# Optimization experiments

Hardware: AMD Instinct MI355X
Metric: run time of the kernel (lower is better)

## Reference

```python
import jax, jax.numpy as jnp
import numpy as np

EMBED_DIM = 1024
N_HEADS = 16
KV_SIZE = 64
CLIP_DIST = 10
SLEN = 1024
BSZ = 8


def setup_inputs() -> dict:
    key = jax.random.key(0)
    ks = jax.random.split(key, 7)
    s = 0.02
    inputs = jax.random.normal(ks[0], (SLEN, BSZ, EMBED_DIM), dtype=jnp.float32)
    W_in = jax.random.normal(ks[1], (3 * N_HEADS * KV_SIZE, EMBED_DIM), dtype=jnp.float32) * s
    b_in = jnp.zeros((3 * N_HEADS * KV_SIZE,), dtype=jnp.float32)
    k_dist_emb = jax.random.normal(ks[2], (CLIP_DIST + 1, KV_SIZE), dtype=jnp.float32) * s
    v_dist_emb = jax.random.normal(ks[3], (CLIP_DIST + 1, KV_SIZE), dtype=jnp.float32) * s
    W_out = jax.random.normal(ks[4], (EMBED_DIM, N_HEADS * KV_SIZE), dtype=jnp.float32) * s
    b_out = jnp.zeros((EMBED_DIM,), dtype=jnp.float32)
    return {"inputs": inputs, "W_in": W_in, "b_in": b_in,
            "k_dist_emb": k_dist_emb, "v_dist_emb": v_dist_emb,
            "W_out": W_out, "b_out": b_out}


def reference(inputs, W_in, b_in, k_dist_emb, v_dist_emb, W_out, b_out):
    slen, bsz, _ = inputs.shape
    h, d = N_HEADS, KV_SIZE
    # in_proj: (slen, bsz, 3*h*d) -> (3, bsz, h, slen, d)
    qkv = inputs @ W_in.T + b_in
    qkv = qkv.reshape(slen, bsz, 3, h, d).transpose(2, 1, 3, 0, 4)
    q, k, v = qkv[0], qkv[1], qkv[2]
    q = q * (d ** -0.5)
    # clipped absolute relative distances (slen, slen)
    idx = jnp.arange(slen)
    dist = jnp.minimum(jnp.abs(idx[None, :] - idx[:, None]), CLIP_DIST)
    k_dist = k_dist_emb[dist]  # (slen, slen, d)
    v_dist = v_dist_emb[dist]  # (slen, slen, d)
    # content scores + relative-distance bias
    attn = jnp.einsum('bhsd,bhtd->bhst', q, k) + jnp.einsum('bhsd,std->bhst', q, k_dist)
    attn = jax.nn.softmax(attn, axis=-1)
    # value accumulation + relative-distance value correction
    out = jnp.einsum('bhst,bhtd->bhsd', attn, v) + jnp.einsum('bhst,std->bhsd', attn, v_dist)
    # (bsz, h, slen, d) -> (slen, bsz, h*d)
    out = out.transpose(2, 0, 1, 3).reshape(slen, bsz, h * d)
    return out @ W_out.T + b_out
```

## Files before the change

kernel.cpp:

```cpp
#include <hip/hip_runtime.h>
#include <hip/hip_bf16.h>
#include <cstdint>


typedef __attribute__((ext_vector_type(8))) __bf16 bf16x8;
typedef __attribute__((ext_vector_type(4))) __bf16 bf16x4;
typedef __attribute__((ext_vector_type(4))) short s16x4;
typedef __attribute__((ext_vector_type(4))) float f32x4;

#if __has_builtin(__builtin_amdgcn_exp2f)
#define EXP2F(x) __builtin_amdgcn_exp2f(x)
#else
#define EXP2F(x) exp2f(x)
#endif

#if __has_builtin(__builtin_amdgcn_mfma_f32_16x16x16bf16_1k)
#define PV_MFMA(ACC, AV, BV) \
  ACC = __builtin_amdgcn_mfma_f32_16x16x16bf16_1k( \
      __builtin_bit_cast(s16x4, AV), __builtin_bit_cast(s16x4, BV), ACC, 0, 0, 0)
#elif __has_builtin(__builtin_amdgcn_mfma_f32_16x16x16_bf16)
#define PV_MFMA(ACC, AV, BV) \
  ACC = __builtin_amdgcn_mfma_f32_16x16x16_bf16(AV, BV, ACC, 0, 0, 0)
#else
#define PV_MFMA(ACC, AV, BV)                                               \
  asm volatile("s_nop 1\n\tv_mfma_f32_16x16x16_bf16 %0, %1, %2, %0\n\t"    \
               "s_nop 7\n\ts_nop 7"                                        \
               : "+v"(ACC)                                                 \
               : "v"(__builtin_bit_cast(s16x4, AV)),                       \
                 "v"(__builtin_bit_cast(s16x4, BV)))
#endif

__device__ __forceinline__ void gload_lds16(const void* g, void* l) {
  __builtin_amdgcn_global_load_lds(
      (const __attribute__((address_space(1))) void*)g,
      (__attribute__((address_space(3))) void*)l, 16, 0, 0);
}

__global__ __launch_bounds__(256) void f2b3_kernel(
    const float* __restrict__ s0, __bf16* __restrict__ d0,
    const float* __restrict__ s1, __bf16* __restrict__ d1,
    const float* __restrict__ s2, __bf16* __restrict__ d2) {
  int i = (blockIdx.x * 256 + threadIdx.x) * 8;
  const float* s; __bf16* d; int off;
  if (i < 8388608) { s = s0; d = d0; off = i; }
  else if (i < 11534336) { s = s1; d = d1; off = i - 8388608; }
  else { s = s2; d = d2; off = i - 11534336; }
  float4 a = *(const float4*)(s + off);
  float4 b = *(const float4*)(s + off + 4);
  bf16x8 o;
  o[0] = (__bf16)a.x; o[1] = (__bf16)a.y; o[2] = (__bf16)a.z; o[3] = (__bf16)a.w;
  o[4] = (__bf16)b.x; o[5] = (__bf16)b.y; o[6] = (__bf16)b.z; o[7] = (__bf16)b.w;
  *(bf16x8*)(d + off) = o;
}

template <int EPI>
__global__ __launch_bounds__(256) void gemm_nt(
    const __bf16* __restrict__ A, const __bf16* __restrict__ B,
    const float* __restrict__ bias, int K,
    float* __restrict__ outF, __bf16* __restrict__ outT, int N, int NT, int CPX) {
  __shared__ __align__(16) __bf16 sA[2][128 * 64];
  __shared__ __align__(16) __bf16 sB[2][128 * 64];
  const int tid = threadIdx.x;
  const int wave = tid >> 6, lane = tid & 63;
  const int lg = lane >> 4, lr = lane & 15;
  const int wr = wave >> 1, wc = wave & 1;
  const int lid = (blockIdx.x & 7) * CPX + (blockIdx.x >> 3);
  const int m0 = (lid / NT) * 128;
  const int n0 = (lid % NT) * 128;

#define STAGE_G(BUF, KT)                                                    \
  _Pragma("unroll") for (int it = 0; it < 4; ++it) {                        \
    int c = it * 256 + tid;                                                 \
    int r = c >> 3, c8 = (c & 7) * 8;                                       \
    gload_lds16(A + (size_t)(m0 + r) * K + (KT) + c8,                       \
                (void*)&sA[BUF][(it * 256 + wave * 64) * 8]);               \
    gload_lds16(B + (size_t)(n0 + r) * K + (KT) + c8,                       \
                (void*)&sB[BUF][(it * 256 + wave * 64) * 8]);               \
  }

  f32x4 acc[4][4] = {};

  STAGE_G(0, 0)
  int buf = 0;
  for (int kt = 0; kt < K; kt += 64) {
    if (kt + 64 < K) {
      STAGE_G(buf ^ 1, kt + 64)
      asm volatile("s_waitcnt vmcnt(8)" ::: "memory");
    } else {
      asm volatile("s_waitcnt vmcnt(0)" ::: "memory");
    }
    __builtin_amdgcn_s_barrier();
#pragma unroll
    for (int kk = 0; kk < 2; ++kk) {
      bf16x8 af[4], bfr[4];
#pragma unroll
      for (int i = 0; i < 4; ++i)
        af[i] = *(const bf16x8*)&sA[buf][(wr * 64 + i * 16 + lr) * 64 + kk * 32 + lg * 8];
#pragma unroll
      for (int j = 0; j < 4; ++j)
        bfr[j] = *(const bf16x8*)&sB[buf][(wc * 64 + j * 16 + lr) * 64 + kk * 32 + lg * 8];
#pragma unroll
      for (int i = 0; i < 4; ++i)
#pragma unroll
        for (int j = 0; j < 4; ++j)
          acc[i][j] = __builtin_amdgcn_mfma_f32_16x16x32_bf16(af[i], bfr[j], acc[i][j], 0, 0, 0);
    }
    __builtin_amdgcn_s_barrier();
    buf ^= 1;
  }
#undef STAGE_G

#pragma unroll
  for (int i = 0; i < 4; ++i) {
    const int gm0 = m0 + wr * 64 + i * 16 + lg * 4;
#pragma unroll
    for (int j = 0; j < 4; ++j) {
      const int gn = n0 + wc * 64 + j * 16 + lr;
      const float bv = bias[gn];
#pragma unroll
      for (int rg = 0; rg < 4; ++rg) {
        const int gm = gm0 + rg;
        float v = acc[i][j][rg] + bv;
        if constexpr (EPI == 0) {
          int t = gn >> 10, h = (gn >> 6) & 15, d = gn & 63;
          int s = gm >> 3, b = gm & 7;
          if (t == 0) v *= 0.18033688011112042f;
          outT[(((size_t)((t * 8 + b) * 16 + h) * 1024 + s) << 6) + d] = (__bf16)v;
        } else {
          outF[(size_t)gm * N + gn] = v;
        }
      }
    }
  }
}

__global__ __launch_bounds__(256) void vtrans_kernel(const __bf16* __restrict__ v,
                                                     __bf16* __restrict__ vt) {
  __shared__ __bf16 tile[64][66];
  const int tid = threadIdx.x;
  const int bh = blockIdx.x >> 4;
  const int s0 = (blockIdx.x & 15) * 64;
  const __bf16* src = v + ((size_t)bh * 1024 + s0) * 64;
#pragma unroll
  for (int it = 0; it < 4; ++it) {
    int idx = it * 256 + tid;
    int r = idx >> 4, c4 = (idx & 15) * 4;
    bf16x4 x = *(const bf16x4*)&src[r * 64 + c4];
    tile[r][c4 + 0] = x[0]; tile[r][c4 + 1] = x[1];
    tile[r][c4 + 2] = x[2]; tile[r][c4 + 3] = x[3];
  }
  __syncthreads();
  __bf16* dst = vt + (size_t)bh * 65536;
#pragma unroll
  for (int it = 0; it < 4; ++it) {
    int idx = it * 256 + tid;
    int dr = idx >> 4, s4 = (idx & 15) * 4;
    bf16x4 y;
    y[0] = tile[s4 + 0][dr]; y[1] = tile[s4 + 1][dr];
    y[2] = tile[s4 + 2][dr]; y[3] = tile[s4 + 3][dr];
    *(bf16x4*)&dst[(size_t)dr * 1024 + s0 + s4] = y;
  }
}

#define ATTN_TILE(KT, KC, KS, VC, VS)                                           \
  {                                                                             \
    if ((KT) < 15)                                                              \
      gload_lds16(vtp + (size_t)srow * 1024 + ((KT) + 1) * 64 + sc8,            \
                  &sV[VS][wave * 512]);                                         \
    if ((KT) < 14)                                                              \
      gload_lds16(kp + (size_t)((KT) * 64 + 128 + srow) * 64 + sc8,             \
                  &sK[KS][wave * 512]);                                         \
    f32x4 sf[4];                                                                \
    __builtin_amdgcn_s_setprio(1);                                              \
    _Pragma("unroll") for (int tj = 0; tj < 4; ++tj) {                          \
      const int t = tj * 16 + lr;                                               \
      bf16x8 bk0 = *(const bf16x8*)&sK[KC][t * 64 + ((lg ^ (t & 7)) * 8)];      \
      bf16x8 bk1 = *(const bf16x8*)&sK[KC][t * 64 + (((4 + lg) ^ (t & 7)) * 8)];\
      f32x4 z = {};                                                             \
      z = __builtin_amdgcn_mfma_f32_16x16x32_bf16(bk0, aq[0], z, 0, 0, 0);      \
      z = __builtin_amdgcn_mfma_f32_16x16x32_bf16(bk1, aq[1], z, 0, 0, 0);      \
      sf[tj] = z;                                                               \
    }                                                                           \
    __builtin_amdgcn_s_setprio(0);                                              \
    const bool inband = ((KT) * 64 <= sb + 24) && ((KT) * 64 + 63 >= sb - 9);   \
    if (inband) {                                                               \
      const float* bDrow = &sBD[wave][lr][0];                                   \
      _Pragma("unroll") for (int tj = 0; tj < 4; ++tj) {                        \
        _Pragma("unroll") for (int rg = 0; rg < 4; ++rg) {                      \
          const int t = (KT) * 64 + tj * 16 + lg * 4 + rg;                      \
          const int dd = t - s;                                                 \
          const int ad = dd < 0 ? -dd : dd;                                     \
          if (ad <= 9) {                                                        \
            const float val = sf[tj][rg] + bDrow[ad];                           \
            sf[tj][rg] = val;                                                   \
            band[wave][lr][dd + 9] = (__bf16)val;                               \
          }                                                                     \
        }                                                                       \
      }                                                                         \
    }                                                                           \
    float vm[4];                                                                \
    _Pragma("unroll") for (int tj = 0; tj < 4; ++tj)                            \
      vm[tj] = fmaxf(fmaxf(sf[tj][0], sf[tj][1]), fmaxf(sf[tj][2], sf[tj][3])); \
    float vmax = fmaxf(fmaxf(vm[0], vm[1]), fmaxf(vm[2], vm[3]));               \
    vmax = fmaxf(vmax, __shfl_xor(vmax, 16, 64));                               \
    vmax = fmaxf(vmax, __shfl_xor(vmax, 32, 64));                               \
    if (__any(vmax > m + 8.f)) {                                                \
      const float mn = fmaxf(m, vmax);                                          \
      const float scl = EXP2F(m - mn);                                          \
      m = mn;                                                                   \
      l *= scl;                                                                 \
      _Pragma("unroll") for (int dj = 0; dj < 4; ++dj)                          \
        _Pragma("unroll") for (int rg = 0; rg < 4; ++rg)                        \
          o_acc[dj][rg] *= scl;                                                 \
    }                                                                           \
    float rs[4];                                                                \
    _Pragma("unroll") for (int tj = 0; tj < 4; ++tj) {                          \
      float p0 = EXP2F(sf[tj][0] - m), p1 = EXP2F(sf[tj][1] - m);               \
      float p2 = EXP2F(sf[tj][2] - m), p3 = EXP2F(sf[tj][3] - m);               \
      sf[tj][0] = p0; sf[tj][1] = p1; sf[tj][2] = p2; sf[tj][3] = p3;           \
      rs[tj] = (p0 + p1) + (p2 + p3);                                           \
    }                                                                           \
    float rsum = (rs[0] + rs[1]) + (rs[2] + rs[3]);                             \
    rsum += __shfl_xor(rsum, 16, 64);                                           \
    rsum += __shfl_xor(rsum, 32, 64);                                           \
    l += rsum;                                                                  \
    bf16x4 pbv[4];                                                              \
    _Pragma("unroll") for (int tj = 0; tj < 4; ++tj) {                          \
      pbv[tj][0] = (__bf16)sf[tj][0]; pbv[tj][1] = (__bf16)sf[tj][1];           \
      pbv[tj][2] = (__bf16)sf[tj][2]; pbv[tj][3] = (__bf16)sf[tj][3];           \
    }                                                                           \
    __builtin_amdgcn_s_setprio(1);                                              \
    _Pragma("unroll") for (int tj = 0; tj < 4; ++tj) {                          \
      _Pragma("unroll") for (int dj = 0; dj < 4; ++dj) {                        \
        const int d = dj * 16 + lr;                                             \
        const int ch = (2 * tj + (lg >> 1)) ^ (d & 7);                          \
        const bf16x4 av = *(const bf16x4*)&sV[VC][d * 64 + ch * 8 + (lg & 1) * 4]; \
        PV_MFMA(o_acc[dj], av, pbv[tj]);                                        \
      }                                                                         \
    }                                                                           \
    __builtin_amdgcn_s_setprio(0);                                              \
    if ((KT) < 14) {                                                            \
      asm volatile("s_waitcnt vmcnt(1)" ::: "memory");                          \
    } else if ((KT) == 14) {                                                    \
      asm volatile("s_waitcnt vmcnt(0)" ::: "memory");                          \
    }                                                                           \
    if ((KT) < 15) __builtin_amdgcn_s_barrier();                                \
  }

__global__ __launch_bounds__(512) void attn_kernel(
    const __bf16* __restrict__ qkv, const __bf16* __restrict__ vt,
    const float* __restrict__ kde, const float* __restrict__ vde,
    __bf16* __restrict__ O) {
  __shared__ __align__(16) __bf16 sK[3][4096];
  __shared__ __align__(16) __bf16 sV[2][4096];
  __shared__ __bf16 band[8][16][20];
  __shared__ float sBD[8][16][10];
  const int tid = threadIdx.x, wave = tid >> 6, lane = tid & 63;
  const int lg = lane >> 4, lr = lane & 15;
  const int lid = (blockIdx.x & 7) * 128 + (blockIdx.x >> 3);
  const int bh = lid >> 3;
  const int stile = lid & 7;
  const int sb = stile * 128 + wave * 16;
  const int b = bh >> 4, h = bh & 15;
  const __bf16* qp = qkv + (size_t)bh * 65536;
  const __bf16* kp = qkv + (size_t)(128 + bh) * 65536;
  const __bf16* vtp = vt + (size_t)bh * 65536;

  const int srow = tid >> 3;
  const int sc8 = ((tid & 7) ^ (srow & 7)) * 8;

  gload_lds16(kp + (size_t)srow * 64 + sc8, &sK[0][wave * 512]);
  gload_lds16(vtp + (size_t)srow * 1024 + sc8, &sV[0][wave * 512]);
  gload_lds16(kp + (size_t)(64 + srow) * 64 + sc8, &sK[1][wave * 512]);

  {
    __bf16* bf = &band[0][0][0];
    for (int i = tid; i < 8 * 16 * 20; i += 512) bf[i] = (__bf16)(-1e30f);
  }

  bf16x8 aq[2];
#pragma unroll
  for (int kk = 0; kk < 2; ++kk)
    aq[kk] = *(const bf16x8*)&qp[(size_t)(sb + lr) * 64 + kk * 32 + lg * 8];

  {
    float kd10[16];
#pragma unroll
    for (int e = 0; e < 16; ++e)
      kd10[e] = kde[640 + (e >> 3) * 32 + lg * 8 + (e & 7)];
#pragma unroll
    for (int c = 0; c < 10; ++c) {
      float acc = 0.f;
#pragma unroll
      for (int e = 0; e < 16; ++e)
        acc += (float)aq[e >> 3][e & 7] *
               (kde[c * 64 + (e >> 3) * 32 + lg * 8 + (e & 7)] - kd10[e]);
      acc += __shfl_xor(acc, 16, 64);
      acc += __shfl_xor(acc, 32, 64);
      if (lg == 0) sBD[wave][lr][c] = acc;
    }
  }

  f32x4 o_acc[4] = {};
  float m = -1e30f, l = 0.f;
  const int s = sb + lr;

  asm volatile("s_waitcnt vmcnt(1)" ::: "memory");
  __builtin_amdgcn_s_barrier();

  ATTN_TILE( 0, 0, 2, 0, 1)
  ATTN_TILE( 1, 1, 0, 1, 0)
  ATTN_TILE( 2, 2, 1, 0, 1)
  ATTN_TILE( 3, 0, 2, 1, 0)
  ATTN_TILE( 4, 1, 0, 0, 1)
  ATTN_TILE( 5, 2, 1, 1, 0)
  ATTN_TILE( 6, 0, 2, 0, 1)
  ATTN_TILE( 7, 1, 0, 1, 0)
  ATTN_TILE( 8, 2, 1, 0, 1)
  ATTN_TILE( 9, 0, 2, 1, 0)
  ATTN_TILE(10, 1, 0, 0, 1)
  ATTN_TILE(11, 2, 1, 1, 0)
  ATTN_TILE(12, 0, 2, 0, 1)
  ATTN_TILE(13, 1, 0, 1, 0)
  ATTN_TILE(14, 2, 1, 0, 1)
  ATTN_TILE(15, 0, 2, 1, 0)

  const float inv = 1.f / l;
  float psum[10];
  psum[0] = EXP2F((float)band[wave][lr][9] - m);
#pragma unroll
  for (int c = 1; c < 10; ++c)
    psum[c] = EXP2F((float)band[wave][lr][9 - c] - m) +
              EXP2F((float)band[wave][lr][9 + c] - m);
#pragma unroll
  for (int dj = 0; dj < 4; ++dj) {
    bf16x4 ov;
#pragma unroll
    for (int rg = 0; rg < 4; ++rg) {
      const int d = dj * 16 + lg * 4 + rg;
      float acc2 = 0.f;
#pragma unroll
      for (int c = 0; c < 10; ++c)
        acc2 += psum[c] * (vde[c * 64 + d] - vde[640 + d]);
      ov[rg] = (__bf16)((o_acc[dj][rg] + acc2) * inv + vde[640 + d]);
    }
    *(bf16x4*)&O[((size_t)(s * 8 + b)) * 1024 + h * 64 + dj * 16 + lg * 4] = ov;
  }
}

extern "C" void kernel_launch(void* const* d_in, const int* in_sizes, int n_in,
                              void* d_out, int out_size, void* d_ws, size_t ws_size,
                              hipStream_t stream) {
  (void)in_sizes; (void)n_in; (void)out_size; (void)ws_size;
  const float* inputs = (const float*)d_in[0];
  const float* W_in   = (const float*)d_in[1];
  const float* b_in   = (const float*)d_in[2];
  const float* kde    = (const float*)d_in[3];
  const float* vde    = (const float*)d_in[4];
  const float* W_out  = (const float*)d_in[5];
  const float* b_out  = (const float*)d_in[6];
  float* out = (float*)d_out;

  char* ws = (char*)d_ws;
  __bf16* qkvt  = (__bf16*)(ws);
  __bf16* vt    = (__bf16*)(ws + 50331648);
  __bf16* Xb    = (__bf16*)(ws + 75497472);
  __bf16* Ob    = (__bf16*)(ws + 75497472);
  __bf16* Wb_in = (__bf16*)(ws + 92274688);
  __bf16* Wb_out= (__bf16*)(ws + 98566144);

  f2b3_kernel<<<6144, 256, 0, stream>>>(inputs, Xb, W_in, Wb_in, W_out, Wb_out);

  gemm_nt<0><<<1536, 256, 0, stream>>>(Xb, Wb_in, b_in, 1024, nullptr, qkvt, 3072, 24, 192);
  vtrans_kernel<<<2048, 256, 0, stream>>>(qkvt + (size_t)2 * 128 * 65536, vt);
  attn_kernel<<<1024, 512, 0, stream>>>(qkvt, vt, kde, vde, Ob);
  gemm_nt<1><<<512, 256, 0, stream>>>(Ob, Wb_out, b_out, 1024, out, nullptr, 1024, 8, 64);
}
```

Before: 202.8 us.

## Replace projection GEMMs with 8-wave 256x128 triple-buffered swizzled-LDS pipeline

Replaces the 4-wave 128x128 double-buffered GEMM with an 8-wave kernel that computes a 256x128 tile. The K loop is fully unrolled over three LDS stages, and global-to-LDS loads are interleaved across four MFMA phases with raised wave priority. LDS columns are XOR-swizzled to avoid bank conflicts on the fragment reads. The aim is to hide global load latency and raise MFMA utilisation for both projection GEMMs, at the cost of a hardcoded K=1024, higher LDS use (144KB), and half as many blocks.

```diff
diff --git a/kernel.cpp b/kernel.cpp
--- a/kernel.cpp
+++ b/kernel.cpp
@@ -53,74 +53,105 @@
   *(bf16x8*)(d + off) = o;
 }
 
+
+#define STG8A(SL, TK, G)                                                      \
+  gload_lds16(A + (size_t)(m0 + (G) * 64 + (tid >> 3)) * K + (TK) * 64 + sgc, \
+              (void*)&sG[SL][(G) * 4096 + wave * 512]);
+#define STG8B(SL, TK, G)                                                      \
+  gload_lds16(Bp + (size_t)(n0 + (G) * 64 + (tid >> 3)) * K + (TK) * 64 + sgc,\
+              (void*)&sG[SL][16384 + (G) * 4096 + wave * 512]);
+
+#define GPH(SL, MP, NP, STAGE_STMT, TAIL_STMT)                                  \
+  {                                                                             \
+    bf16x8 af[2][2], bfr[2][2];                                                 \
+    _Pragma("unroll") for (int mi = 0; mi < 2; ++mi)                            \
+      _Pragma("unroll") for (int kk = 0; kk < 2; ++kk)                          \
+        af[mi][kk] = *(const bf16x8*)&sG[SL][                                   \
+            (wr * 64 + ((MP) * 2 + mi) * 16 + lr) * 64 +                        \
+            (((kk * 4 + lg) ^ (lr & 7)) * 8)];                                  \
+    _Pragma("unroll") for (int ni = 0; ni < 2; ++ni)                            \
+      _Pragma("unroll") for (int kk = 0; kk < 2; ++kk)                          \
+        bfr[ni][kk] = *(const bf16x8*)&sG[SL][16384 +                           \
+            (wc * 64 + ((NP) * 2 + ni) * 16 + lr) * 64 +                        \
+            (((kk * 4 + lg) ^ (lr & 7)) * 8)];                                  \
+    STAGE_STMT                                                                  \
+    __builtin_amdgcn_s_barrier();                                               \
+    asm volatile("s_waitcnt lgkmcnt(0)" ::: "memory");                          \
+    __builtin_amdgcn_sched_barrier(0);                                          \
+    __builtin_amdgcn_s_setprio(1);                                              \
+    _Pragma("unroll") for (int mi = 0; mi < 2; ++mi)                            \
+      _Pragma("unroll") for (int ni = 0; ni < 2; ++ni)                          \
+        _Pragma("unroll") for (int kk = 0; kk < 2; ++kk)                        \
+          acc[(MP) * 2 + mi][(NP) * 2 + ni] =                                   \
+              __builtin_amdgcn_mfma_f32_16x16x32_bf16(                          \
+                  af[mi][kk], bfr[ni][kk],                                      \
+                  acc[(MP) * 2 + mi][(NP) * 2 + ni], 0, 0, 0);                  \
+    __builtin_amdgcn_s_setprio(0);                                              \
+    TAIL_STMT                                                                   \
+    __builtin_amdgcn_s_barrier();                                               \
+  }
+
+#define GTILE(SL, SS, TK2, DOSTG, WAITC)                                        \
+  GPH(SL, 0, 0, if (DOSTG) { STG8A(SS, TK2, 0) STG8A(SS, TK2, 1) }, )           \
+  GPH(SL, 0, 1, if (DOSTG) { STG8A(SS, TK2, 2) STG8A(SS, TK2, 3) }, )           \
+  GPH(SL, 1, 0, if (DOSTG) { STG8B(SS, TK2, 0) }, )                             \
+  GPH(SL, 1, 1, if (DOSTG) { STG8B(SS, TK2, 1) },                               \
+      if ((WAITC) == 6) { asm volatile("s_waitcnt vmcnt(6)" ::: "memory"); }    \
+      else if ((WAITC) == 0) { asm volatile("s_waitcnt vmcnt(0)" ::: "memory"); })
+
 template <int EPI>
-__global__ __launch_bounds__(256) void gemm_nt(
-    const __bf16* __restrict__ A, const __bf16* __restrict__ B,
+__global__ __launch_bounds__(512) void gemm8p(
+    const __bf16* __restrict__ A, const __bf16* __restrict__ Bp,
     const float* __restrict__ bias, int K,
     float* __restrict__ outF, __bf16* __restrict__ outT, int N, int NT, int CPX) {
-  __shared__ __align__(16) __bf16 sA[2][128 * 64];
-  __shared__ __align__(16) __bf16 sB[2][128 * 64];
+  __shared__ __align__(16) __bf16 sG[3][24576];
   const int tid = threadIdx.x;
   const int wave = tid >> 6, lane = tid & 63;
   const int lg = lane >> 4, lr = lane & 15;
   const int wr = wave >> 1, wc = wave & 1;
   const int lid = (blockIdx.x & 7) * CPX + (blockIdx.x >> 3);
-  const int m0 = (lid / NT) * 128;
+  const int m0 = (lid / NT) * 256;
   const int n0 = (lid % NT) * 128;
 
-#define STAGE_G(BUF, KT)                                                    \
-  _Pragma("unroll") for (int it = 0; it < 4; ++it) {                        \
-    int c = it * 256 + tid;                                                 \
-    int r = c >> 3, c8 = (c & 7) * 8;                                       \
-    gload_lds16(A + (size_t)(m0 + r) * K + (KT) + c8,                       \
-                (void*)&sA[BUF][(it * 256 + wave * 64) * 8]);               \
-    gload_lds16(B + (size_t)(n0 + r) * K + (KT) + c8,                       \
-                (void*)&sB[BUF][(it * 256 + wave * 64) * 8]);               \
-  }
+  const int sgc = ((tid & 7) ^ ((tid >> 3) & 7)) * 8;
 
   f32x4 acc[4][4] = {};
 
-  STAGE_G(0, 0)
-  int buf = 0;
-  for (int kt = 0; kt < K; kt += 64) {
-    if (kt + 64 < K) {
-      STAGE_G(buf ^ 1, kt + 64)
-      asm volatile("s_waitcnt vmcnt(8)" ::: "memory");
-    } else {
-      asm volatile("s_waitcnt vmcnt(0)" ::: "memory");
-    }
-    __builtin_amdgcn_s_barrier();
-#pragma unroll
-    for (int kk = 0; kk < 2; ++kk) {
-      bf16x8 af[4], bfr[4];
-#pragma unroll
-      for (int i = 0; i < 4; ++i)
-        af[i] = *(const bf16x8*)&sA[buf][(wr * 64 + i * 16 + lr) * 64 + kk * 32 + lg * 8];
-#pragma unroll
-      for (int j = 0; j < 4; ++j)
-        bfr[j] = *(const bf16x8*)&sB[buf][(wc * 64 + j * 16 + lr) * 64 + kk * 32 + lg * 8];
-#pragma unroll
-      for (int i = 0; i < 4; ++i)
-#pragma unroll
-        for (int j = 0; j < 4; ++j)
-          acc[i][j] = __builtin_amdgcn_mfma_f32_16x16x32_bf16(af[i], bfr[j], acc[i][j], 0, 0, 0);
-    }
-    __builtin_amdgcn_s_barrier();
-    buf ^= 1;
-  }
-#undef STAGE_G
-
-#pragma unroll
-  for (int i = 0; i < 4; ++i) {
-    const int gm0 = m0 + wr * 64 + i * 16 + lg * 4;
-#pragma unroll
-    for (int j = 0; j < 4; ++j) {
-      const int gn = n0 + wc * 64 + j * 16 + lr;
+  STG8A(0, 0, 0) STG8A(0, 0, 1) STG8A(0, 0, 2) STG8A(0, 0, 3)
+  STG8B(0, 0, 0) STG8B(0, 0, 1)
+  STG8A(1, 1, 0) STG8A(1, 1, 1) STG8A(1, 1, 2) STG8A(1, 1, 3)
+  STG8B(1, 1, 0) STG8B(1, 1, 1)
+  asm volatile("s_waitcnt vmcnt(6)" ::: "memory");
+  __builtin_amdgcn_s_barrier();
+
+  GTILE(0, 2, 2, 1, 6)
+  GTILE(1, 0, 3, 1, 6)
+  GTILE(2, 1, 4, 1, 6)
+  GTILE(0, 2, 5, 1, 6)
+  GTILE(1, 0, 6, 1, 6)
+  GTILE(2, 1, 7, 1, 6)
+  GTILE(0, 2, 8, 1, 6)
+  GTILE(1, 0, 9, 1, 6)
+  GTILE(2, 1, 10, 1, 6)
+  GTILE(0, 2, 11, 1, 6)
+  GTILE(1, 0, 12, 1, 6)
+  GTILE(2, 1, 13, 1, 6)
+  GTILE(0, 2, 14, 1, 6)
+  GTILE(1, 0, 15, 1, 6)
+  GTILE(2, 1, 16, 0, 0)
+  GTILE(0, 2, 17, 0, 2)
+
+#pragma unroll
+  for (int mf = 0; mf < 4; ++mf) {
+    const int gm0 = m0 + wr * 64 + mf * 16 + lg * 4;
+#pragma unroll
+    for (int nf = 0; nf < 4; ++nf) {
+      const int gn = n0 + wc * 64 + nf * 16 + lr;
       const float bv = bias[gn];
 #pragma unroll
       for (int rg = 0; rg < 4; ++rg) {
         const int gm = gm0 + rg;
-        float v = acc[i][j][rg] + bv;
+        float v = acc[mf][nf][rg] + bv;
         if constexpr (EPI == 0) {
           int t = gn >> 10, h = (gn >> 6) & 15, d = gn & 63;
           int s = gm >> 3, b = gm & 7;
@@ -371,8 +402,8 @@
 
   f2b3_kernel<<<6144, 256, 0, stream>>>(inputs, Xb, W_in, Wb_in, W_out, Wb_out);
 
-  gemm_nt<0><<<1536, 256, 0, stream>>>(Xb, Wb_in, b_in, 1024, nullptr, qkvt, 3072, 24, 192);
+  gemm8p<0><<<768, 512, 0, stream>>>(Xb, Wb_in, b_in, 1024, nullptr, qkvt, 3072, 24, 96);
   vtrans_kernel<<<2048, 256, 0, stream>>>(qkvt + (size_t)2 * 128 * 65536, vt);
   attn_kernel<<<1024, 512, 0, stream>>>(qkvt, vt, kde, vde, Ob);
-  gemm_nt<1><<<512, 256, 0, stream>>>(Ob, Wb_out, b_out, 1024, out, nullptr, 1024, 8, 64);
-}
+  gemm8p<1><<<256, 512, 0, stream>>>(Ob, Wb_out, b_out, 1024, out, nullptr, 1024, 8, 32);
+}
```

Measured after the change: 197.6 us. -2.6%, faster.
